# Kernel optimization log

Hardware: AMD Instinct MI355X
Metric: run time of the kernel (lower is better)

The kernel has to match this reference:

```python
import jax, jax.numpy as jnp
import numpy as np
from jax import lax

SEQ_LEN, BATCH, Z_DIM, X_DIM = 512, 256, 64, 10000


def setup_inputs() -> dict:
    key = jax.random.key(0)
    k1, k2, k3, k4 = jax.random.split(key, 4)
    inp = jax.random.randint(k1, (SEQ_LEN, BATCH), 0, X_DIM)
    # Row-stochastic transition matrix so probability mass is conserved by alpha @ T.T
    T = jax.random.uniform(k2, (Z_DIM, Z_DIM), dtype=jnp.float32)
    T = T / T.sum(axis=1, keepdims=True)
    pi = jax.random.uniform(k3, (Z_DIM,), dtype=jnp.float32)
    pi = pi / pi.sum()
    # Emission weights near 1.0 so the unnormalized recursion stays in fp32 range
    emit = 0.7 + 0.6 * jax.random.uniform(k4, (X_DIM, Z_DIM), dtype=jnp.float32)
    return {"input": inp, "T": T, "pi": pi, "emit": emit}


def reference(input, T, pi, emit):
    # input: [S, B] int; emit: [X, Z]; T: [Z, Z]; pi: [Z]
    e = emit[input]                      # [S, B, Z] gather of emission weights
    alpha0 = e[0] * pi[None, :]          # [B, Z]

    def fwd_step(a_prev, e_t):
        a_t = e_t * (a_prev @ T.T)       # [B, Z]
        return a_t, a_t

    _, alphas = lax.scan(fwd_step, alpha0, e[1:])
    alpha = jnp.concatenate([alpha0[None], alphas], axis=0)  # [S, B, Z]

    beta_last = jnp.ones_like(alpha0)    # beta[S-1] = 1

    def bwd_step(b_next, e_t1):
        b_t = (e_t1 * b_next) @ T        # [B, Z]
        return b_t, b_t

    # xs[t] = e[t+1]; reverse scan yields beta[t] for t = 0..S-2 in order
    _, betas = lax.scan(bwd_step, beta_last, e[1:], reverse=True)
    beta = jnp.concatenate([betas, beta_last[None]], axis=0)  # [S, B, Z]

    ab = alpha * beta
    posterior_marginal = ab / ab.sum(-1, keepdims=True)
    return alpha, beta, posterior_marginal
```

## Files before the change

### kernel.cpp

```cpp
#include <hip/hip_runtime.h>
#include <hip/hip_bf16.h>

#define SEQ   512
#define BATCH 256
#define ZD    64

__device__ __forceinline__ float lane_bcastf(float v, int i) {
  return __int_as_float(__builtin_amdgcn_readlane(__float_as_int(v), i));
}
__device__ __forceinline__ int lane_bcasti(int v, int i) {
  return __builtin_amdgcn_readlane(v, i);
}

#define REP8(M,p)  M(p##0) M(p##1) M(p##2) M(p##3) M(p##4) M(p##5) M(p##6) M(p##7)
#define REP64(M)   REP8(M,0) REP8(M,1) REP8(M,2) REP8(M,3) \
                   REP8(M,4) REP8(M,5) REP8(M,6) REP8(M,7)

#define TDECL(n)  float t##n;
#define TLOADF(n) t##n = Trp[0##n];
#define TLOADB(n) t##n = Tcp[(0##n) * ZD];
#define TFMA(n)   acc[(0##n) & 3] = fmaf(lane_bcastf(vbc, 0##n), t##n, acc[(0##n) & 3]);
#define TPIN(p)   asm volatile("" : "+v"(t##p##0), "+v"(t##p##1), "+v"(t##p##2), \
                                    "+v"(t##p##3), "+v"(t##p##4), "+v"(t##p##5), \
                                    "+v"(t##p##6), "+v"(t##p##7));
#define TPIN_ALL  TPIN(0) TPIN(1) TPIN(2) TPIN(3) TPIN(4) TPIN(5) TPIN(6) TPIN(7)

__global__ __launch_bounds__(64, 1) void hmm_chains(
    const int*   __restrict__ inp,
    const float* __restrict__ T,
    const float* __restrict__ pi,
    const float* __restrict__ emit,
    float* __restrict__ out_alpha,
    float* __restrict__ out_beta)
{
  const int lane = threadIdx.x;
  const int blk  = blockIdx.x;
  const bool fwd = (blk < BATCH);
  const int b    = fwd ? blk : blk - BATCH;

  int xv[8];
  #pragma unroll
  for (int w = 0; w < 8; ++w)
    xv[w] = inp[(w * 64 + lane) * BATCH + b];

  REP64(TDECL)

  if (fwd) {
    const float* Trp = T + lane * ZD;
    REP64(TLOADF)
    TPIN_ALL

    const int x0 = lane_bcasti(xv[0], 0);
    float alpha = emit[x0 * ZD + lane] * pi[lane];
    float* op = out_alpha + (size_t)b * ZD + lane;
    *op = alpha;
    op += BATCH * ZD;

    #pragma unroll
    for (int w = 0; w < 8; ++w) {
      const int xvw = xv[w];
      #pragma unroll 1
      for (int idx = (w == 0) ? 1 : 0; idx < 64; ++idx) {
        const int   xt = lane_bcasti(xvw, idx);
        const float e  = emit[xt * ZD + lane];
        float acc[4] = {0.f, 0.f, 0.f, 0.f};
        const float vbc = alpha;
        REP64(TFMA)
        alpha = e * ((acc[0] + acc[1]) + (acc[2] + acc[3]));
        *op = alpha;
        op += BATCH * ZD;
      }
    }
  } else {
    const float* Tcp = T + lane;
    REP64(TLOADB)
    TPIN_ALL

    float beta = 1.0f;
    float* op = out_beta + ((size_t)(SEQ - 1) * BATCH + b) * ZD + lane;
    *op = beta;
    op -= BATCH * ZD;

    const int xL = lane_bcasti(xv[7], 63);
    float e_next = emit[xL * ZD + lane];

    #pragma unroll
    for (int w = 7; w >= 0; --w) {
      const int xvw = xv[w];
      #pragma unroll 1
      for (int idx = (w == 7) ? 62 : 63; idx >= 0; --idx) {
        const int   xt   = lane_bcasti(xvw, idx);
        const float e_pf = emit[xt * ZD + lane];
        const float vbc  = e_next * beta;
        float acc[4] = {0.f, 0.f, 0.f, 0.f};
        REP64(TFMA)
        beta = (acc[0] + acc[1]) + (acc[2] + acc[3]);
        *op = beta;
        op -= BATCH * ZD;
        e_next = e_pf;
      }
    }
  }
}

__global__ __launch_bounds__(256) void posterior_k(
    const float* __restrict__ a,
    const float* __restrict__ bt,
    float*       __restrict__ p)
{
  const int tid = blockIdx.x * 256 + threadIdx.x;
  const size_t base = (size_t)tid * 8;

  const float4 va0 = *reinterpret_cast<const float4*>(a  + base);
  const float4 va1 = *reinterpret_cast<const float4*>(a  + base + 4);
  const float4 vb0 = *reinterpret_cast<const float4*>(bt + base);
  const float4 vb1 = *reinterpret_cast<const float4*>(bt + base + 4);

  const float p0 = va0.x * vb0.x;
  const float p1 = va0.y * vb0.y;
  const float p2 = va0.z * vb0.z;
  const float p3 = va0.w * vb0.w;
  const float p4 = va1.x * vb1.x;
  const float p5 = va1.y * vb1.y;
  const float p6 = va1.z * vb1.z;
  const float p7 = va1.w * vb1.w;

  float s = ((p0 + p1) + (p2 + p3)) + ((p4 + p5) + (p6 + p7));
  s += __shfl_xor(s, 1);
  s += __shfl_xor(s, 2);
  s += __shfl_xor(s, 4);
  const float inv = 1.0f / s;

  float4 o0, o1;
  o0.x = p0 * inv; o0.y = p1 * inv; o0.z = p2 * inv; o0.w = p3 * inv;
  o1.x = p4 * inv; o1.y = p5 * inv; o1.z = p6 * inv; o1.w = p7 * inv;
  *reinterpret_cast<float4*>(p + base)     = o0;
  *reinterpret_cast<float4*>(p + base + 4) = o1;
}

extern "C" void kernel_launch(void* const* d_in, const int* in_sizes, int n_in,
                              void* d_out, int out_size, void* d_ws, size_t ws_size,
                              hipStream_t stream) {
  const int*   inp  = (const int*)  d_in[0];
  const float* T    = (const float*)d_in[1];
  const float* pi   = (const float*)d_in[2];
  const float* emit = (const float*)d_in[3];

  float* out = (float*)d_out;
  const size_t N = (size_t)SEQ * BATCH * ZD;
  float* out_alpha = out;
  float* out_beta  = out + N;
  float* out_post  = out + 2 * N;

  hipLaunchKernelGGL(hmm_chains, dim3(2 * BATCH), dim3(64), 0, stream,
                     inp, T, pi, emit, out_alpha, out_beta);

  hipLaunchKernelGGL(posterior_k, dim3((unsigned)(N / 2048)), dim3(256), 0, stream,
                     out_alpha, out_beta, out_post);
}
```

Measured before the change: 240.4 us.

## Prefetch emission rows two steps ahead and process two rows per posterior thread

The forward and backward recurrences now load emission rows two timesteps ahead instead of one, using pre-shifted index vectors, so each gather has an extra iteration to hide its global-memory latency behind the 64-FMA chain. The posterior kernel handles two elements per thread (one in each half of the sequence), halving the grid size and increasing memory-level parallelism. The costs are a few more registers and extra index loads per chain.

```diff
diff --git a/kernel.cpp b/kernel.cpp
--- a/kernel.cpp
+++ b/kernel.cpp
@@ -38,40 +38,58 @@
   const bool fwd = (blk < BATCH);
   const int b    = fwd ? blk : blk - BATCH;
 
-  int xv[8];
-  #pragma unroll
-  for (int w = 0; w < 8; ++w)
-    xv[w] = inp[(w * 64 + lane) * BATCH + b];
-
   REP64(TDECL)
 
   if (fwd) {
+    int xvn[8], xvn2[8];
+    #pragma unroll
+    for (int w = 0; w < 8; ++w) {
+      int li1 = w * 64 + lane + 1; if (li1 > SEQ - 1) li1 = SEQ - 1;
+      int li2 = w * 64 + lane + 2; if (li2 > SEQ - 1) li2 = SEQ - 1;
+      xvn[w]  = inp[li1 * BATCH + b];
+      xvn2[w] = inp[li2 * BATCH + b];
+    }
+
     const float* Trp = T + lane * ZD;
     REP64(TLOADF)
     TPIN_ALL
 
-    const int x0 = lane_bcasti(xv[0], 0);
+    const int x0 = inp[b];
     float alpha = emit[x0 * ZD + lane] * pi[lane];
     float* op = out_alpha + (size_t)b * ZD + lane;
     *op = alpha;
     op += BATCH * ZD;
 
+    const int x1 = lane_bcasti(xvn[0], 0);
+    float e_cur = emit[x1 * ZD + lane];
+    const int x2 = lane_bcasti(xvn2[0], 0);
+    float e_nx  = emit[x2 * ZD + lane];
+
     #pragma unroll
     for (int w = 0; w < 8; ++w) {
-      const int xvw = xv[w];
+      const int xn2w = xvn2[w];
       #pragma unroll 1
       for (int idx = (w == 0) ? 1 : 0; idx < 64; ++idx) {
-        const int   xt = lane_bcasti(xvw, idx);
-        const float e  = emit[xt * ZD + lane];
+        const int   xt2  = lane_bcasti(xn2w, idx);
+        const float e_pf = emit[xt2 * ZD + lane];
         float acc[4] = {0.f, 0.f, 0.f, 0.f};
         const float vbc = alpha;
         REP64(TFMA)
-        alpha = e * ((acc[0] + acc[1]) + (acc[2] + acc[3]));
+        alpha = e_cur * ((acc[0] + acc[1]) + (acc[2] + acc[3]));
         *op = alpha;
         op += BATCH * ZD;
+        e_cur = e_nx;
+        e_nx  = e_pf;
       }
     }
   } else {
+    int xvm[8];
+    #pragma unroll
+    for (int w = 0; w < 8; ++w) {
+      int li = w * 64 + lane - 1; if (li < 0) li = 0;
+      xvm[w] = inp[li * BATCH + b];
+    }
+
     const float* Tcp = T + lane;
     REP64(TLOADB)
     TPIN_ALL
@@ -81,23 +99,26 @@
     *op = beta;
     op -= BATCH * ZD;
 
-    const int xL = lane_bcasti(xv[7], 63);
-    float e_next = emit[xL * ZD + lane];
+    const int xL  = inp[(SEQ - 1) * BATCH + b];
+    const int xL1 = inp[(SEQ - 2) * BATCH + b];
+    float e_next = emit[xL  * ZD + lane];
+    float e_n2   = emit[xL1 * ZD + lane];
 
     #pragma unroll
     for (int w = 7; w >= 0; --w) {
-      const int xvw = xv[w];
+      const int xmw = xvm[w];
       #pragma unroll 1
       for (int idx = (w == 7) ? 62 : 63; idx >= 0; --idx) {
-        const int   xt   = lane_bcasti(xvw, idx);
-        const float e_pf = emit[xt * ZD + lane];
+        const int   xtm  = lane_bcasti(xmw, idx);
+        const float e_pf = emit[xtm * ZD + lane];
         const float vbc  = e_next * beta;
         float acc[4] = {0.f, 0.f, 0.f, 0.f};
         REP64(TFMA)
         beta = (acc[0] + acc[1]) + (acc[2] + acc[3]);
         *op = beta;
         op -= BATCH * ZD;
-        e_next = e_pf;
+        e_next = e_n2;
+        e_n2   = e_pf;
       }
     }
   }
@@ -109,33 +130,45 @@
     float*       __restrict__ p)
 {
   const int tid = blockIdx.x * 256 + threadIdx.x;
-  const size_t base = (size_t)tid * 8;
+  const size_t base  = (size_t)tid * 8;
+  const size_t base2 = base + (size_t)(SEQ / 2) * BATCH * ZD;
 
   const float4 va0 = *reinterpret_cast<const float4*>(a  + base);
   const float4 va1 = *reinterpret_cast<const float4*>(a  + base + 4);
   const float4 vb0 = *reinterpret_cast<const float4*>(bt + base);
   const float4 vb1 = *reinterpret_cast<const float4*>(bt + base + 4);
+  const float4 wa0 = *reinterpret_cast<const float4*>(a  + base2);
+  const float4 wa1 = *reinterpret_cast<const float4*>(a  + base2 + 4);
+  const float4 wb0 = *reinterpret_cast<const float4*>(bt + base2);
+  const float4 wb1 = *reinterpret_cast<const float4*>(bt + base2 + 4);
 
-  const float p0 = va0.x * vb0.x;
-  const float p1 = va0.y * vb0.y;
-  const float p2 = va0.z * vb0.z;
-  const float p3 = va0.w * vb0.w;
-  const float p4 = va1.x * vb1.x;
-  const float p5 = va1.y * vb1.y;
-  const float p6 = va1.z * vb1.z;
-  const float p7 = va1.w * vb1.w;
+  const float p0 = va0.x * vb0.x, p1 = va0.y * vb0.y;
+  const float p2 = va0.z * vb0.z, p3 = va0.w * vb0.w;
+  const float p4 = va1.x * vb1.x, p5 = va1.y * vb1.y;
+  const float p6 = va1.z * vb1.z, p7 = va1.w * vb1.w;
+
+  const float q0 = wa0.x * wb0.x, q1 = wa0.y * wb0.y;
+  const float q2 = wa0.z * wb0.z, q3 = wa0.w * wb0.w;
+  const float q4 = wa1.x * wb1.x, q5 = wa1.y * wb1.y;
+  const float q6 = wa1.z * wb1.z, q7 = wa1.w * wb1.w;
 
   float s = ((p0 + p1) + (p2 + p3)) + ((p4 + p5) + (p6 + p7));
-  s += __shfl_xor(s, 1);
-  s += __shfl_xor(s, 2);
-  s += __shfl_xor(s, 4);
-  const float inv = 1.0f / s;
+  float u = ((q0 + q1) + (q2 + q3)) + ((q4 + q5) + (q6 + q7));
+  s += __shfl_xor(s, 1);  u += __shfl_xor(u, 1);
+  s += __shfl_xor(s, 2);  u += __shfl_xor(u, 2);
+  s += __shfl_xor(s, 4);  u += __shfl_xor(u, 4);
+  const float inv  = 1.0f / s;
+  const float inv2 = 1.0f / u;
 
-  float4 o0, o1;
-  o0.x = p0 * inv; o0.y = p1 * inv; o0.z = p2 * inv; o0.w = p3 * inv;
-  o1.x = p4 * inv; o1.y = p5 * inv; o1.z = p6 * inv; o1.w = p7 * inv;
-  *reinterpret_cast<float4*>(p + base)     = o0;
-  *reinterpret_cast<float4*>(p + base + 4) = o1;
+  float4 o0, o1, o2, o3;
+  o0.x = p0 * inv;  o0.y = p1 * inv;  o0.z = p2 * inv;  o0.w = p3 * inv;
+  o1.x = p4 * inv;  o1.y = p5 * inv;  o1.z = p6 * inv;  o1.w = p7 * inv;
+  o2.x = q0 * inv2; o2.y = q1 * inv2; o2.z = q2 * inv2; o2.w = q3 * inv2;
+  o3.x = q4 * inv2; o3.y = q5 * inv2; o3.z = q6 * inv2; o3.w = q7 * inv2;
+  *reinterpret_cast<float4*>(p + base)      = o0;
+  *reinterpret_cast<float4*>(p + base + 4)  = o1;
+  *reinterpret_cast<float4*>(p + base2)     = o2;
+  *reinterpret_cast<float4*>(p + base2 + 4) = o3;
 }
 
 extern "C" void kernel_launch(void* const* d_in, const int* in_sizes, int n_in,
@@ -155,6 +188,6 @@
   hipLaunchKernelGGL(hmm_chains, dim3(2 * BATCH), dim3(64), 0, stream,
                      inp, T, pi, emit, out_alpha, out_beta);
 
-  hipLaunchKernelGGL(posterior_k, dim3((unsigned)(N / 2048)), dim3(256), 0, stream,
+  hipLaunchKernelGGL(posterior_k, dim3((unsigned)(N / 2 / 2048)), dim3(256), 0, stream,
                      out_alpha, out_beta, out_post);
 }
```

Result: slower. 247.8 us (+3.1%).

## Fuse posterior pass into chain kernel via cooperative grid sync

Applied to the files above, without the earlier changes.

Merges the forward/backward chain kernel and the posterior normalization kernel into one cooperative launch. After a grid-wide barrier, each of the 512 single-wave blocks loops over its share of the alpha*beta normalization. This removes one kernel launch and its gap. The cost is a grid sync, cooperative-launch overhead, and a posterior phase that runs on only 512 wavefronts instead of a wide grid.

```diff
diff --git a/kernel.cpp b/kernel.cpp
--- a/kernel.cpp
+++ b/kernel.cpp
@@ -1,5 +1,8 @@
 #include <hip/hip_runtime.h>
 #include <hip/hip_bf16.h>
+#include <hip/hip_cooperative_groups.h>
+
+namespace cg = cooperative_groups;
 
 #define SEQ   512
 #define BATCH 256
@@ -25,13 +28,14 @@
                                     "+v"(t##p##6), "+v"(t##p##7));
 #define TPIN_ALL  TPIN(0) TPIN(1) TPIN(2) TPIN(3) TPIN(4) TPIN(5) TPIN(6) TPIN(7)
 
-__global__ __launch_bounds__(64, 1) void hmm_chains(
+__global__ __launch_bounds__(64, 1) void hmm_fused(
     const int*   __restrict__ inp,
     const float* __restrict__ T,
     const float* __restrict__ pi,
     const float* __restrict__ emit,
     float* __restrict__ out_alpha,
-    float* __restrict__ out_beta)
+    float* __restrict__ out_beta,
+    float* __restrict__ out_post)
 {
   const int lane = threadIdx.x;
   const int blk  = blockIdx.x;
@@ -101,41 +105,41 @@
       }
     }
   }
-}
 
-__global__ __launch_bounds__(256) void posterior_k(
-    const float* __restrict__ a,
-    const float* __restrict__ bt,
-    float*       __restrict__ p)
-{
-  const int tid = blockIdx.x * 256 + threadIdx.x;
-  const size_t base = (size_t)tid * 8;
+  cg::this_grid().sync();
 
-  const float4 va0 = *reinterpret_cast<const float4*>(a  + base);
-  const float4 va1 = *reinterpret_cast<const float4*>(a  + base + 4);
-  const float4 vb0 = *reinterpret_cast<const float4*>(bt + base);
-  const float4 vb1 = *reinterpret_cast<const float4*>(bt + base + 4);
+  const int gtid = blk * 64 + lane;
+  #pragma unroll 1
+  for (int it = 0; it < (SEQ * BATCH * ZD / 8) / (2 * BATCH * 64); ++it) {
+    const size_t slot = (size_t)it * (2 * BATCH * 64) + gtid;
+    const size_t base = slot * 8;
 
-  const float p0 = va0.x * vb0.x;
-  const float p1 = va0.y * vb0.y;
-  const float p2 = va0.z * vb0.z;
-  const float p3 = va0.w * vb0.w;
-  const float p4 = va1.x * vb1.x;
-  const float p5 = va1.y * vb1.y;
-  const float p6 = va1.z * vb1.z;
-  const float p7 = va1.w * vb1.w;
+    const float4 va0 = *reinterpret_cast<const float4*>(out_alpha + base);
+    const float4 va1 = *reinterpret_cast<const float4*>(out_alpha + base + 4);
+    const float4 vb0 = *reinterpret_cast<const float4*>(out_beta  + base);
+    const float4 vb1 = *reinterpret_cast<const float4*>(out_beta  + base + 4);
 
-  float s = ((p0 + p1) + (p2 + p3)) + ((p4 + p5) + (p6 + p7));
-  s += __shfl_xor(s, 1);
-  s += __shfl_xor(s, 2);
-  s += __shfl_xor(s, 4);
-  const float inv = 1.0f / s;
+    const float p0 = va0.x * vb0.x;
+    const float p1 = va0.y * vb0.y;
+    const float p2 = va0.z * vb0.z;
+    const float p3 = va0.w * vb0.w;
+    const float p4 = va1.x * vb1.x;
+    const float p5 = va1.y * vb1.y;
+    const float p6 = va1.z * vb1.z;
+    const float p7 = va1.w * vb1.w;
 
-  float4 o0, o1;
-  o0.x = p0 * inv; o0.y = p1 * inv; o0.z = p2 * inv; o0.w = p3 * inv;
-  o1.x = p4 * inv; o1.y = p5 * inv; o1.z = p6 * inv; o1.w = p7 * inv;
-  *reinterpret_cast<float4*>(p + base)     = o0;
-  *reinterpret_cast<float4*>(p + base + 4) = o1;
+    float s = ((p0 + p1) + (p2 + p3)) + ((p4 + p5) + (p6 + p7));
+    s += __shfl_xor(s, 1);
+    s += __shfl_xor(s, 2);
+    s += __shfl_xor(s, 4);
+    const float inv = 1.0f / s;
+
+    float4 o0, o1;
+    o0.x = p0 * inv; o0.y = p1 * inv; o0.z = p2 * inv; o0.w = p3 * inv;
+    o1.x = p4 * inv; o1.y = p5 * inv; o1.z = p6 * inv; o1.w = p7 * inv;
+    *reinterpret_cast<float4*>(out_post + base)     = o0;
+    *reinterpret_cast<float4*>(out_post + base + 4) = o1;
+  }
 }
 
 extern "C" void kernel_launch(void* const* d_in, const int* in_sizes, int n_in,
@@ -152,9 +156,8 @@
   float* out_beta  = out + N;
   float* out_post  = out + 2 * N;
 
-  hipLaunchKernelGGL(hmm_chains, dim3(2 * BATCH), dim3(64), 0, stream,
-                     inp, T, pi, emit, out_alpha, out_beta);
-
-  hipLaunchKernelGGL(posterior_k, dim3((unsigned)(N / 2048)), dim3(256), 0, stream,
-                     out_alpha, out_beta, out_post);
+  void* args[] = {(void*)&inp, (void*)&T, (void*)&pi, (void*)&emit,
+                  (void*)&out_alpha, (void*)&out_beta, (void*)&out_post};
+  hipLaunchCooperativeKernel(reinterpret_cast<const void*>(hmm_fused),
+                             dim3(2 * BATCH), dim3(64), args, 0, stream);
 }
```

New measurement: 334.8 us. 1.39x slower.
